# Optimization experiments

Hardware: AMD Instinct MI355X
Metric: run time of the kernel (lower is better)

## Reference

```python
import jax, jax.numpy as jnp
import numpy as np

B, S, D, H = 2, 2048, 1024, 16
HD = D // H
EPS = 1e-5


def setup_inputs() -> dict:
    key = jax.random.key(0)
    ks = jax.random.split(key, 11)
    sc = 0.02
    return {
        "x": jax.random.normal(ks[0], (B, S, D), jnp.float32),
        "wq": jax.random.normal(ks[1], (D, D), jnp.float32) * sc,
        "bq": jax.random.normal(ks[2], (D,), jnp.float32) * sc,
        "wk": jax.random.normal(ks[3], (D, D), jnp.float32) * sc,
        "bk": jax.random.normal(ks[4], (D,), jnp.float32) * sc,
        "wv": jax.random.normal(ks[5], (D, D), jnp.float32) * sc,
        "bv": jax.random.normal(ks[6], (D,), jnp.float32) * sc,
        "wo": jax.random.normal(ks[7], (D, D), jnp.float32) * sc,
        "bo": jax.random.normal(ks[8], (D,), jnp.float32) * sc,
        "gamma": 1.0 + jax.random.normal(ks[9], (D,), jnp.float32) * sc,
        "beta": jax.random.normal(ks[10], (D,), jnp.float32) * sc,
    }


def _layernorm(x, gamma, beta):
    mu = jnp.mean(x, axis=-1, keepdims=True)
    var = jnp.mean(jnp.square(x - mu), axis=-1, keepdims=True)
    return (x - mu) * jax.lax.rsqrt(var + EPS) * gamma + beta


def reference(x, wq, bq, wk, bk, wv, bv, wo, bo, gamma, beta):
    h = _layernorm(x, gamma, beta)
    # projections; torch Linear: y = x @ W.T + b
    q = (h @ wq.T + bq).reshape(B, S, H, HD).transpose(0, 2, 1, 3)  # [B,H,S,HD]
    k = (h @ wk.T + bk).reshape(B, S, H, HD).transpose(0, 2, 1, 3)
    v = (h @ wv.T + bv).reshape(B, S, H, HD).transpose(0, 2, 1, 3)
    # NOTE: original divides by sqrt(d_dim), not sqrt(head_dim)
    scores = jnp.einsum("bhqd,bhkd->bhqk", q, k) / np.sqrt(D).astype(np.float32)
    # faithful quirky causal masking: triu->transpose->softmax(dim=-2)->triu->transpose
    t = jnp.triu(scores).swapaxes(-2, -1)
    p = jax.nn.softmax(t, axis=-2)
    a = jnp.triu(p).swapaxes(-2, -1)  # [B,H,S,S]
    attn = jnp.einsum("bhqk,bhkd->bhqd", a, v)
    concat = attn.transpose(0, 2, 1, 3).reshape(B, S, D)
    return x + concat @ wo.T + bo
```

## Files before the change

kernel.cpp:

```cpp
#include <hip/hip_runtime.h>
#include <stdint.h>

typedef unsigned short u16;
typedef __bf16 bf8 __attribute__((ext_vector_type(8)));
typedef float f4 __attribute__((ext_vector_type(4)));

#define S_ 2048
#define D_ 1024
#define H_ 16
#define HD_ 64
#define M_ 4096

__device__ __forceinline__ u16 f2bf(float f) {
  union { float f; uint32_t u; } v; v.f = f;
  uint32_t u = v.u;
  u += 0x7FFF + ((u >> 16) & 1);
  return (u16)(u >> 16);
}

__device__ __forceinline__ float fexp2(float x) {
#if __has_builtin(__builtin_amdgcn_exp2f)
  return __builtin_amdgcn_exp2f(x);
#else
  float r; asm("v_exp_f32 %0, %1" : "=v"(r) : "v"(x)); return r;
#endif
}

__device__ __forceinline__ void load_lds16(const void* g, void* l) {
  __builtin_amdgcn_global_load_lds(
      (const __attribute__((address_space(1))) void*)g,
      (__attribute__((address_space(3))) void*)l, 16, 0, 0);
}

__device__ __forceinline__ void stage_ab(
    const u16* __restrict__ A, const u16* __restrict__ B,
    int m0, int n0, int kt, u16* buf, int tid) {
  #pragma unroll
  for (int l = 0; l < 4; ++l) {
    int p = l * 256 + tid;
    int q = p & 511;
    int row = q >> 2, c = q & 3;
    int clog = c ^ ((row >> 1) & 3);
    const u16* src = (p >> 9)
        ? (B + (size_t)(n0 + row) * 1024 + kt * 32 + clog * 8)
        : (A + (size_t)(m0 + row) * 1024 + kt * 32 + clog * 8);
    load_lds16(src, buf + p * 8);
  }
}

__global__ __launch_bounds__(256) void ln_kernel(
    const float* __restrict__ x, const float* __restrict__ gamma,
    const float* __restrict__ beta, u16* __restrict__ hbf) {
  int row = blockIdx.x;
  int tid = threadIdx.x;
  int w = tid >> 6, lane = tid & 63;
  const float* xr = x + (size_t)row * D_;
  float lv[4];
  float s = 0.f;
  #pragma unroll
  for (int i = 0; i < 4; ++i) { lv[i] = xr[tid + i * 256]; s += lv[i]; }
  __shared__ float red[8];
  #pragma unroll
  for (int off = 32; off >= 1; off >>= 1) s += __shfl_xor(s, off);
  if (lane == 0) red[w] = s;
  __syncthreads();
  float mean = (red[0] + red[1] + red[2] + red[3]) * (1.f / D_);
  float vs = 0.f;
  #pragma unroll
  for (int i = 0; i < 4; ++i) { float d = lv[i] - mean; vs += d * d; }
  #pragma unroll
  for (int off = 32; off >= 1; off >>= 1) vs += __shfl_xor(vs, off);
  if (lane == 0) red[4 + w] = vs;
  __syncthreads();
  float var = (red[4] + red[5] + red[6] + red[7]) * (1.f / D_);
  float rstd = rsqrtf(var + 1e-5f);
  #pragma unroll
  for (int i = 0; i < 4; ++i) {
    int col = tid + i * 256;
    float y = (lv[i] - mean) * rstd * gamma[col] + beta[col];
    hbf[(size_t)row * D_ + col] = f2bf(y);
  }
}

__global__ __launch_bounds__(256) void convw_kernel(
    const float* __restrict__ wq, const float* __restrict__ wk,
    const float* __restrict__ wv, const float* __restrict__ wo,
    u16* __restrict__ wqkv, u16* __restrict__ wobf, float* __restrict__ Z) {
  int i4 = blockIdx.x * 256 + threadIdx.x;
  int base = i4 * 4;
  int part = base >> 20;
  int off = base & 0xFFFFF;
  const float* src = part == 0 ? wq : part == 1 ? wk : part == 2 ? wv : wo;
  float4 v = *(const float4*)(src + off);
  ushort4 o;
  o.x = f2bf(v.x); o.y = f2bf(v.y); o.z = f2bf(v.z); o.w = f2bf(v.w);
  if (part < 3) *(ushort4*)(wqkv + base) = o;
  else *(ushort4*)(wobf + off) = o;
  if (i4 < 32 * S_) Z[i4] = (float)(i4 & (S_ - 1));
}

__global__ __launch_bounds__(256, 2) void gemm_qkv_kernel(
    const u16* __restrict__ A,
    const u16* __restrict__ W,
    const float* __restrict__ bq, const float* __restrict__ bk,
    const float* __restrict__ bv,
    u16* __restrict__ Qb, u16* __restrict__ Kb, float* __restrict__ Vf) {
  __shared__ u16 smem[4 * 8192];
  const int tid = threadIdx.x;
  const int w = tid >> 6, lane = tid & 63;
  const int wr = w >> 1, wc = w & 1;
  const int lr = lane & 15, hi = lane >> 4;
  const int kswz = (hi ^ ((lr >> 1) & 3)) * 8;

  int bid = blockIdx.x;
  int swz = (bid & 7) * 96 + (bid >> 3);
  const int m0 = (swz & 31) * 128;
  const int n0 = (swz >> 5) * 128;

  f4 acc[4][4];
  f4 zero = {0.f, 0.f, 0.f, 0.f};
  #pragma unroll
  for (int i = 0; i < 4; ++i)
    #pragma unroll
    for (int j = 0; j < 4; ++j) acc[i][j] = zero;

  stage_ab(A, W, m0, n0, 0, smem, tid);
  stage_ab(A, W, m0, n0, 1, smem + 8192, tid);
  stage_ab(A, W, m0, n0, 2, smem + 16384, tid);

  for (int t = 0; t < 32; ++t) {
    if (t < 30)      asm volatile("s_waitcnt vmcnt(8)\n\ts_barrier" ::: "memory");
    else if (t == 30) asm volatile("s_waitcnt vmcnt(4)\n\ts_barrier" ::: "memory");
    else             asm volatile("s_waitcnt vmcnt(0)\n\ts_barrier" ::: "memory");
    const u16* As = smem + (t & 3) * 8192;
    const u16* Bs = As + 4096;
    bf8 av[4], bvv[4];
    #pragma unroll
    for (int i = 0; i < 4; ++i)
      av[i] = *(const bf8*)&As[(wr * 64 + i * 16 + lr) * 32 + kswz];
    #pragma unroll
    for (int j = 0; j < 4; ++j)
      bvv[j] = *(const bf8*)&Bs[(wc * 64 + j * 16 + lr) * 32 + kswz];
    if (t < 29) stage_ab(A, W, m0, n0, t + 3, smem + ((t + 3) & 3) * 8192, tid);
    __builtin_amdgcn_s_setprio(1);
    #pragma unroll
    for (int i = 0; i < 4; ++i)
      #pragma unroll
      for (int j = 0; j < 4; ++j)
        acc[i][j] = __builtin_amdgcn_mfma_f32_16x16x32_bf16(
            av[i], bvv[j], acc[i][j], 0, 0, 0);
    __builtin_amdgcn_s_setprio(0);
  }

  const int part = n0 >> 10;
  const int colbase = n0 & 1023;
  const float SCQ = 0.04508422002778011f;
  if (part == 0) {
    #pragma unroll
    for (int i = 0; i < 4; ++i)
      #pragma unroll
      for (int j = 0; j < 4; ++j)
        #pragma unroll
        for (int r = 0; r < 4; ++r) {
          int m = m0 + wr * 64 + i * 16 + hi * 4 + r;
          int col = colbase + wc * 64 + j * 16 + lr;
          float val = (acc[i][j][r] + bq[col]) * SCQ;
          int b = m >> 11, s = m & 2047;
          int hh = col >> 6, d = col & 63;
          Qb[((size_t)(b * H_ + hh) * S_ + s) * HD_ + d] = f2bf(val);
        }
  } else if (part == 1) {
    #pragma unroll
    for (int i = 0; i < 4; ++i)
      #pragma unroll
      for (int j = 0; j < 4; ++j)
        #pragma unroll
        for (int r = 0; r < 4; ++r) {
          int m = m0 + wr * 64 + i * 16 + hi * 4 + r;
          int col = colbase + wc * 64 + j * 16 + lr;
          float val = acc[i][j][r] + bk[col];
          int b = m >> 11, s = m & 2047;
          int hh = col >> 6, d = col & 63;
          Kb[((size_t)(b * H_ + hh) * S_ + s) * HD_ + d] = f2bf(val);
        }
  } else {
    #pragma unroll
    for (int i = 0; i < 4; ++i)
      #pragma unroll
      for (int j = 0; j < 4; ++j)
        #pragma unroll
        for (int r = 0; r < 4; ++r) {
          int m = m0 + wr * 64 + i * 16 + hi * 4 + r;
          int col = colbase + wc * 64 + j * 16 + lr;
          float val = acc[i][j][r] + bv[col];
          int b = m >> 11, s = m & 2047;
          int hh = col >> 6, d = col & 63;
          Vf[((size_t)(b * H_ + hh) * S_ + s) * HD_ + d] = val;
        }
  }
}

__global__ __launch_bounds__(256, 4) void scores_z_kernel(
    const u16* __restrict__ Qb, const u16* __restrict__ Kb,
    float* __restrict__ Z, float* __restrict__ Ed) {
  int bid = blockIdx.x;
  int idx = bid >> 3;
  int bh = (bid & 7) * 4 + (idx / 144);
  int t = idx - (idx / 144) * 144;
  int g = 0;
  while (true) { int cnt = 4 * (8 - g); if (t < cnt) break; t -= cnt; ++g; }
  const int qb = g * 4 + (t & 3);
  const int c = g + (t >> 2);
  const bool diag = (c == g);

  const int tid = threadIdx.x;
  const int w = tid >> 6, lane = tid & 63;
  const int lr = lane & 15, hi = lane >> 4, lkb = hi * 8;
  const u16* Qh = Qb + (size_t)bh * S_ * HD_;
  const u16* Kh = Kb + (size_t)bh * S_ * HD_;
  const int q0 = qb * 64;

  bf8 a[4][2];
  #pragma unroll
  for (int g2 = 0; g2 < 4; ++g2) {
    a[g2][0] = *(const bf8*)&Qh[(q0 + g2 * 16 + lr) * 64 + lkb];
    a[g2][1] = *(const bf8*)&Qh[(q0 + g2 * 16 + lr) * 64 + 32 + lkb];
  }
  bf8 kb[4][2];
  #pragma unroll
  for (int i = 0; i < 4; ++i) {
    int kt = c * 16 + w + i * 4;
    kb[i][0] = *(const bf8*)&Kh[(kt * 16 + lr) * 64 + lkb];
    kb[i][1] = *(const bf8*)&Kh[(kt * 16 + lr) * 64 + 32 + lkb];
  }
  __builtin_amdgcn_sched_barrier(0);

  float zacc[4][4];
  #pragma unroll
  for (int g2 = 0; g2 < 4; ++g2)
    #pragma unroll
    for (int r = 0; r < 4; ++r) zacc[g2][r] = 0.f;

  #pragma unroll
  for (int i = 0; i < 4; ++i) {
    int kt = c * 16 + w + i * 4;
    int kcol = kt * 16 + lr;
    f4 cc[4];
    #pragma unroll
    for (int g2 = 0; g2 < 4; ++g2) {
      f4 z4 = {0.f, 0.f, 0.f, 0.f};
      z4 = __builtin_amdgcn_mfma_f32_16x16x32_bf16(a[g2][0], kb[i][0], z4, 0, 0, 0);
      cc[g2] = __builtin_amdgcn_mfma_f32_16x16x32_bf16(a[g2][1], kb[i][1], z4, 0, 0, 0);
    }
    if (diag) {
      #pragma unroll
      for (int g2 = 0; g2 < 4; ++g2) {
        #pragma unroll
        for (int r = 0; r < 4; ++r) {
          float e = fexp2(cc[g2][r]);
          int qrow = q0 + g2 * 16 + hi * 4 + r;
          zacc[g2][r] += (kcol >= qrow) ? e : 0.f;
          if (kcol == qrow) Ed[(size_t)bh * S_ + qrow] = e;
        }
      }
    } else {
      #pragma unroll
      for (int g2 = 0; g2 < 4; ++g2) {
        #pragma unroll
        for (int r = 0; r < 4; ++r)
          zacc[g2][r] += fexp2(cc[g2][r]);
      }
    }
  }

  __shared__ float Zp[4][64];
  #pragma unroll
  for (int g2 = 0; g2 < 4; ++g2) {
    #pragma unroll
    for (int r = 0; r < 4; ++r) {
      float v = zacc[g2][r];
      v += __shfl_xor(v, 1);
      v += __shfl_xor(v, 2);
      v += __shfl_xor(v, 4);
      v += __shfl_xor(v, 8);
      if (lr == 0) Zp[w][g2 * 16 + hi * 4 + r] = v;
    }
  }
  __syncthreads();
  if (tid < 64) {
    float z = Zp[0][tid] + Zp[1][tid] + Zp[2][tid] + Zp[3][tid];
    atomicAdd(&Z[(size_t)bh * S_ + q0 + tid], z);
  }
}

#define NC_ 128

__global__ __launch_bounds__(64) void vchunk_kernel(
    const float* __restrict__ Vf, float* __restrict__ csum) {
  int bh = blockIdx.y, c = blockIdx.x;
  int d = threadIdx.x;
  const float* vp = Vf + ((size_t)bh * S_ + c * 16) * HD_ + d;
  float s = 0.f;
  #pragma unroll
  for (int r = 0; r < 16; ++r) s += vp[r * HD_];
  csum[((size_t)bh * NC_ + c) * HD_ + d] = s;
}

__global__ __launch_bounds__(256) void vprefix_kernel(float* __restrict__ csum) {
  int bh = blockIdx.x;
  int d = threadIdx.x & 63;
  int qt = threadIdx.x >> 6;
  __shared__ float tot[4][64];
  float v[32];
  #pragma unroll
  for (int c = 0; c < 32; ++c)
    v[c] = csum[((size_t)bh * NC_ + qt * 32 + c) * HD_ + d];
  float run = 0.f;
  #pragma unroll
  for (int c = 0; c < 32; ++c) { float t = v[c]; v[c] = run; run += t; }
  tot[qt][d] = run;
  __syncthreads();
  float off = 0.f;
  #pragma unroll
  for (int p = 0; p < 4; ++p) if (p < qt) off += tot[p][d];
  #pragma unroll
  for (int c = 0; c < 32; ++c)
    csum[((size_t)bh * NC_ + qt * 32 + c) * HD_ + d] = v[c] + off;
}

__global__ __launch_bounds__(64) void attn_out_kernel(
    const float* __restrict__ Vf, const float* __restrict__ csum,
    const float* __restrict__ Z, const float* __restrict__ Ed,
    u16* __restrict__ concat) {
  int bh = blockIdx.y, c = blockIdx.x;
  int d = threadIdx.x;
  int b = bh >> 4, h = bh & 15;
  float run = csum[((size_t)bh * NC_ + c) * HD_ + d];
  #pragma unroll
  for (int r = 0; r < 16; ++r) {
    int s = c * 16 + r;
    size_t vi = ((size_t)bh * S_ + s) * HD_ + d;
    float v = Vf[vi];
    float z = Z[(size_t)bh * S_ + s];
    float e = Ed[(size_t)bh * S_ + s];
    float a = (run + e * v) / z;
    concat[(size_t)(b * S_ + s) * D_ + h * HD_ + d] = f2bf(a);
    run += v;
  }
}

__global__ __launch_bounds__(256, 2) void gemm_out_kernel(
    const u16* __restrict__ A,
    const u16* __restrict__ W,
    const float* __restrict__ x, const float* __restrict__ bo,
    float* __restrict__ out) {
  __shared__ u16 smem[4 * 8192];
  const int tid = threadIdx.x;
  const int w = tid >> 6, lane = tid & 63;
  const int wr = w >> 1, wc = w & 1;
  const int lr = lane & 15, hi = lane >> 4;
  const int kswz = (hi ^ ((lr >> 1) & 3)) * 8;

  int bid = blockIdx.x;
  int swz = (bid & 7) * 32 + (bid >> 3);
  const int m0 = (swz & 31) * 128;
  const int n0 = (swz >> 5) * 128;

  f4 acc[4][4];
  f4 zero = {0.f, 0.f, 0.f, 0.f};
  #pragma unroll
  for (int i = 0; i < 4; ++i)
    #pragma unroll
    for (int j = 0; j < 4; ++j) acc[i][j] = zero;

  stage_ab(A, W, m0, n0, 0, smem, tid);
  stage_ab(A, W, m0, n0, 1, smem + 8192, tid);
  stage_ab(A, W, m0, n0, 2, smem + 16384, tid);

  for (int t = 0; t < 32; ++t) {
    if (t < 30)      asm volatile("s_waitcnt vmcnt(8)\n\ts_barrier" ::: "memory");
    else if (t == 30) asm volatile("s_waitcnt vmcnt(4)\n\ts_barrier" ::: "memory");
    else             asm volatile("s_waitcnt vmcnt(0)\n\ts_barrier" ::: "memory");
    const u16* As = smem + (t & 3) * 8192;
    const u16* Bs = As + 4096;
    bf8 av[4], bvv[4];
    #pragma unroll
    for (int i = 0; i < 4; ++i)
      av[i] = *(const bf8*)&As[(wr * 64 + i * 16 + lr) * 32 + kswz];
    #pragma unroll
    for (int j = 0; j < 4; ++j)
      bvv[j] = *(const bf8*)&Bs[(wc * 64 + j * 16 + lr) * 32 + kswz];
    if (t < 29) stage_ab(A, W, m0, n0, t + 3, smem + ((t + 3) & 3) * 8192, tid);
    __builtin_amdgcn_s_setprio(1);
    #pragma unroll
    for (int i = 0; i < 4; ++i)
      #pragma unroll
      for (int j = 0; j < 4; ++j)
        acc[i][j] = __builtin_amdgcn_mfma_f32_16x16x32_bf16(
            av[i], bvv[j], acc[i][j], 0, 0, 0);
    __builtin_amdgcn_s_setprio(0);
  }

  #pragma unroll
  for (int i = 0; i < 4; ++i)
    #pragma unroll
    for (int j = 0; j < 4; ++j)
      #pragma unroll
      for (int r = 0; r < 4; ++r) {
        int m = m0 + wr * 64 + i * 16 + hi * 4 + r;
        int n = n0 + wc * 64 + j * 16 + lr;
        size_t oi = (size_t)m * D_ + n;
        out[oi] = x[oi] + acc[i][j][r] + bo[n];
      }
}

extern "C" void kernel_launch(void* const* d_in, const int* in_sizes, int n_in,
                              void* d_out, int out_size, void* d_ws, size_t ws_size,
                              hipStream_t stream) {
  (void)in_sizes; (void)n_in; (void)out_size; (void)ws_size;
  const float* x     = (const float*)d_in[0];
  const float* wq    = (const float*)d_in[1];
  const float* bq    = (const float*)d_in[2];
  const float* wk    = (const float*)d_in[3];
  const float* bk    = (const float*)d_in[4];
  const float* wv    = (const float*)d_in[5];
  const float* bv    = (const float*)d_in[6];
  const float* wo    = (const float*)d_in[7];
  const float* bo    = (const float*)d_in[8];
  const float* gamma = (const float*)d_in[9];
  const float* beta  = (const float*)d_in[10];
  float* out = (float*)d_out;

  char* ws = (char*)d_ws;
  u16* hbf    = (u16*)(ws);
  u16* wqkv   = (u16*)(ws + (8u << 20));
  u16* wobf   = (u16*)(ws + (14u << 20));
  u16* Qb     = (u16*)(ws + (16u << 20));
  u16* Kb     = (u16*)(ws + (24u << 20));
  float* Vf   = (float*)(ws + (32u << 20));
  float* Z    = (float*)(ws + (48u << 20));
  float* Ed   = (float*)(ws + (48u << 20) + (256u << 10));
  float* csum = (float*)(ws);
  u16* concat = (u16*)(ws + (16u << 20));

  ln_kernel<<<dim3(4096), dim3(256), 0, stream>>>(x, gamma, beta, hbf);
  convw_kernel<<<dim3(4096), dim3(256), 0, stream>>>(wq, wk, wv, wo, wqkv, wobf, Z);
  gemm_qkv_kernel<<<dim3(768), dim3(256), 0, stream>>>(hbf, wqkv, bq, bk, bv,
                                                       Qb, Kb, Vf);
  scores_z_kernel<<<dim3(4608), dim3(256), 0, stream>>>(Qb, Kb, Z, Ed);
  vchunk_kernel<<<dim3(NC_, 32), dim3(64), 0, stream>>>(Vf, csum);
  vprefix_kernel<<<dim3(32), dim3(256), 0, stream>>>(csum);
  attn_out_kernel<<<dim3(NC_, 32), dim3(64), 0, stream>>>(Vf, csum, Z, Ed, concat);
  gemm_out_kernel<<<dim3(256), dim3(256), 0, stream>>>(concat, wobf, x, bo, out);
}
```

Measured before the change: 210.0 us.

## Fuse prep kernels, store V as bf16, and retune GEMM pipelines and tile mapping

Merges the layernorm and weight-conversion kernels into one launch, which removes a kernel boundary. V is now stored as bf16 instead of fp32, halving its write and read traffic in the V-consuming kernels at some cost in precision. Both GEMMs move from a 4-stage to a 3-stage LDS ring with occupancy hint 3, and use a new XCD-aware block-to-tile mapping meant to improve L2 reuse. The shallower prefetch depth may expose more load latency.

```diff
diff --git a/kernel.cpp b/kernel.cpp
--- a/kernel.cpp
+++ b/kernel.cpp
@@ -16,6 +16,10 @@
   uint32_t u = v.u;
   u += 0x7FFF + ((u >> 16) & 1);
   return (u16)(u >> 16);
+}
+
+__device__ __forceinline__ float b2f(u16 u) {
+  union { uint32_t u; float f; } v; v.u = (uint32_t)u << 16; return v.f;
 }
 
 __device__ __forceinline__ float fexp2(float x) {
@@ -48,64 +52,64 @@
   }
 }
 
-__global__ __launch_bounds__(256) void ln_kernel(
+__global__ __launch_bounds__(256) void prep_kernel(
     const float* __restrict__ x, const float* __restrict__ gamma,
-    const float* __restrict__ beta, u16* __restrict__ hbf) {
-  int row = blockIdx.x;
-  int tid = threadIdx.x;
-  int w = tid >> 6, lane = tid & 63;
-  const float* xr = x + (size_t)row * D_;
-  float lv[4];
-  float s = 0.f;
-  #pragma unroll
-  for (int i = 0; i < 4; ++i) { lv[i] = xr[tid + i * 256]; s += lv[i]; }
-  __shared__ float red[8];
-  #pragma unroll
-  for (int off = 32; off >= 1; off >>= 1) s += __shfl_xor(s, off);
-  if (lane == 0) red[w] = s;
-  __syncthreads();
-  float mean = (red[0] + red[1] + red[2] + red[3]) * (1.f / D_);
-  float vs = 0.f;
-  #pragma unroll
-  for (int i = 0; i < 4; ++i) { float d = lv[i] - mean; vs += d * d; }
-  #pragma unroll
-  for (int off = 32; off >= 1; off >>= 1) vs += __shfl_xor(vs, off);
-  if (lane == 0) red[4 + w] = vs;
-  __syncthreads();
-  float var = (red[4] + red[5] + red[6] + red[7]) * (1.f / D_);
-  float rstd = rsqrtf(var + 1e-5f);
-  #pragma unroll
-  for (int i = 0; i < 4; ++i) {
-    int col = tid + i * 256;
-    float y = (lv[i] - mean) * rstd * gamma[col] + beta[col];
-    hbf[(size_t)row * D_ + col] = f2bf(y);
-  }
-}
-
-__global__ __launch_bounds__(256) void convw_kernel(
+    const float* __restrict__ beta, u16* __restrict__ hbf,
     const float* __restrict__ wq, const float* __restrict__ wk,
     const float* __restrict__ wv, const float* __restrict__ wo,
     u16* __restrict__ wqkv, u16* __restrict__ wobf, float* __restrict__ Z) {
-  int i4 = blockIdx.x * 256 + threadIdx.x;
-  int base = i4 * 4;
-  int part = base >> 20;
-  int off = base & 0xFFFFF;
-  const float* src = part == 0 ? wq : part == 1 ? wk : part == 2 ? wv : wo;
-  float4 v = *(const float4*)(src + off);
-  ushort4 o;
-  o.x = f2bf(v.x); o.y = f2bf(v.y); o.z = f2bf(v.z); o.w = f2bf(v.w);
-  if (part < 3) *(ushort4*)(wqkv + base) = o;
-  else *(ushort4*)(wobf + off) = o;
-  if (i4 < 32 * S_) Z[i4] = (float)(i4 & (S_ - 1));
-}
-
-__global__ __launch_bounds__(256, 2) void gemm_qkv_kernel(
+  int tid = threadIdx.x;
+  if (blockIdx.x < 4096) {
+    int row = blockIdx.x;
+    int w = tid >> 6, lane = tid & 63;
+    const float* xr = x + (size_t)row * D_;
+    float lv[4];
+    float s = 0.f;
+    #pragma unroll
+    for (int i = 0; i < 4; ++i) { lv[i] = xr[tid + i * 256]; s += lv[i]; }
+    __shared__ float red[8];
+    #pragma unroll
+    for (int off = 32; off >= 1; off >>= 1) s += __shfl_xor(s, off);
+    if (lane == 0) red[w] = s;
+    __syncthreads();
+    float mean = (red[0] + red[1] + red[2] + red[3]) * (1.f / D_);
+    float vs = 0.f;
+    #pragma unroll
+    for (int i = 0; i < 4; ++i) { float d = lv[i] - mean; vs += d * d; }
+    #pragma unroll
+    for (int off = 32; off >= 1; off >>= 1) vs += __shfl_xor(vs, off);
+    if (lane == 0) red[4 + w] = vs;
+    __syncthreads();
+    float var = (red[4] + red[5] + red[6] + red[7]) * (1.f / D_);
+    float rstd = rsqrtf(var + 1e-5f);
+    #pragma unroll
+    for (int i = 0; i < 4; ++i) {
+      int col = tid + i * 256;
+      float y = (lv[i] - mean) * rstd * gamma[col] + beta[col];
+      hbf[(size_t)row * D_ + col] = f2bf(y);
+    }
+  } else {
+    int i4 = (blockIdx.x - 4096) * 256 + tid;
+    int base = i4 * 4;
+    int part = base >> 20;
+    int off = base & 0xFFFFF;
+    const float* src = part == 0 ? wq : part == 1 ? wk : part == 2 ? wv : wo;
+    float4 v = *(const float4*)(src + off);
+    ushort4 o;
+    o.x = f2bf(v.x); o.y = f2bf(v.y); o.z = f2bf(v.z); o.w = f2bf(v.w);
+    if (part < 3) *(ushort4*)(wqkv + base) = o;
+    else *(ushort4*)(wobf + off) = o;
+    if (i4 < 32 * S_) Z[i4] = (float)(i4 & (S_ - 1));
+  }
+}
+
+__global__ __launch_bounds__(256, 3) void gemm_qkv_kernel(
     const u16* __restrict__ A,
     const u16* __restrict__ W,
     const float* __restrict__ bq, const float* __restrict__ bk,
     const float* __restrict__ bv,
-    u16* __restrict__ Qb, u16* __restrict__ Kb, float* __restrict__ Vf) {
-  __shared__ u16 smem[4 * 8192];
+    u16* __restrict__ Qb, u16* __restrict__ Kb, u16* __restrict__ Vb) {
+  __shared__ u16 smem[3 * 8192];
   const int tid = threadIdx.x;
   const int w = tid >> 6, lane = tid & 63;
   const int wr = w >> 1, wc = w & 1;
@@ -113,91 +117,63 @@
   const int kswz = (hi ^ ((lr >> 1) & 3)) * 8;
 
   int bid = blockIdx.x;
-  int swz = (bid & 7) * 96 + (bid >> 3);
-  const int m0 = (swz & 31) * 128;
-  const int n0 = (swz >> 5) * 128;
+  int xcd = bid & 7, i = bid >> 3;
+  int rc = xcd >> 2, cc = xcd & 3;
+  const int m0 = (rc * 16 + (i & 15)) * 128;
+  const int n0 = (cc * 6 + (i >> 4)) * 128;
 
   f4 acc[4][4];
   f4 zero = {0.f, 0.f, 0.f, 0.f};
   #pragma unroll
-  for (int i = 0; i < 4; ++i)
-    #pragma unroll
-    for (int j = 0; j < 4; ++j) acc[i][j] = zero;
+  for (int i2 = 0; i2 < 4; ++i2)
+    #pragma unroll
+    for (int j = 0; j < 4; ++j) acc[i2][j] = zero;
 
   stage_ab(A, W, m0, n0, 0, smem, tid);
   stage_ab(A, W, m0, n0, 1, smem + 8192, tid);
-  stage_ab(A, W, m0, n0, 2, smem + 16384, tid);
 
   for (int t = 0; t < 32; ++t) {
-    if (t < 30)      asm volatile("s_waitcnt vmcnt(8)\n\ts_barrier" ::: "memory");
-    else if (t == 30) asm volatile("s_waitcnt vmcnt(4)\n\ts_barrier" ::: "memory");
-    else             asm volatile("s_waitcnt vmcnt(0)\n\ts_barrier" ::: "memory");
-    const u16* As = smem + (t & 3) * 8192;
+    if (t < 31) asm volatile("s_waitcnt vmcnt(4)\n\ts_barrier" ::: "memory");
+    else        asm volatile("s_waitcnt vmcnt(0)\n\ts_barrier" ::: "memory");
+    const u16* As = smem + (t % 3) * 8192;
     const u16* Bs = As + 4096;
     bf8 av[4], bvv[4];
     #pragma unroll
-    for (int i = 0; i < 4; ++i)
-      av[i] = *(const bf8*)&As[(wr * 64 + i * 16 + lr) * 32 + kswz];
+    for (int i2 = 0; i2 < 4; ++i2)
+      av[i2] = *(const bf8*)&As[(wr * 64 + i2 * 16 + lr) * 32 + kswz];
     #pragma unroll
     for (int j = 0; j < 4; ++j)
       bvv[j] = *(const bf8*)&Bs[(wc * 64 + j * 16 + lr) * 32 + kswz];
-    if (t < 29) stage_ab(A, W, m0, n0, t + 3, smem + ((t + 3) & 3) * 8192, tid);
+    if (t < 30) stage_ab(A, W, m0, n0, t + 2, smem + ((t + 2) % 3) * 8192, tid);
     __builtin_amdgcn_s_setprio(1);
     #pragma unroll
-    for (int i = 0; i < 4; ++i)
+    for (int i2 = 0; i2 < 4; ++i2)
       #pragma unroll
       for (int j = 0; j < 4; ++j)
-        acc[i][j] = __builtin_amdgcn_mfma_f32_16x16x32_bf16(
-            av[i], bvv[j], acc[i][j], 0, 0, 0);
+        acc[i2][j] = __builtin_amdgcn_mfma_f32_16x16x32_bf16(
+            av[i2], bvv[j], acc[i2][j], 0, 0, 0);
     __builtin_amdgcn_s_setprio(0);
   }
 
   const int part = n0 >> 10;
   const int colbase = n0 & 1023;
   const float SCQ = 0.04508422002778011f;
-  if (part == 0) {
-    #pragma unroll
-    for (int i = 0; i < 4; ++i)
-      #pragma unroll
-      for (int j = 0; j < 4; ++j)
-        #pragma unroll
-        for (int r = 0; r < 4; ++r) {
-          int m = m0 + wr * 64 + i * 16 + hi * 4 + r;
-          int col = colbase + wc * 64 + j * 16 + lr;
-          float val = (acc[i][j][r] + bq[col]) * SCQ;
-          int b = m >> 11, s = m & 2047;
-          int hh = col >> 6, d = col & 63;
-          Qb[((size_t)(b * H_ + hh) * S_ + s) * HD_ + d] = f2bf(val);
-        }
-  } else if (part == 1) {
-    #pragma unroll
-    for (int i = 0; i < 4; ++i)
-      #pragma unroll
-      for (int j = 0; j < 4; ++j)
-        #pragma unroll
-        for (int r = 0; r < 4; ++r) {
-          int m = m0 + wr * 64 + i * 16 + hi * 4 + r;
-          int col = colbase + wc * 64 + j * 16 + lr;
-          float val = acc[i][j][r] + bk[col];
-          int b = m >> 11, s = m & 2047;
-          int hh = col >> 6, d = col & 63;
-          Kb[((size_t)(b * H_ + hh) * S_ + s) * HD_ + d] = f2bf(val);
-        }
-  } else {
-    #pragma unroll
-    for (int i = 0; i < 4; ++i)
-      #pragma unroll
-      for (int j = 0; j < 4; ++j)
-        #pragma unroll
-        for (int r = 0; r < 4; ++r) {
-          int m = m0 + wr * 64 + i * 16 + hi * 4 + r;
-          int col = colbase + wc * 64 + j * 16 + lr;
-          float val = acc[i][j][r] + bv[col];
-          int b = m >> 11, s = m & 2047;
-          int hh = col >> 6, d = col & 63;
-          Vf[((size_t)(b * H_ + hh) * S_ + s) * HD_ + d] = val;
-        }
-  }
+  const float* bias_p = part == 0 ? bq : (part == 1 ? bk : bv);
+  u16* dst = part == 0 ? Qb : (part == 1 ? Kb : Vb);
+  const float scale = part == 0 ? SCQ : 1.f;
+  #pragma unroll
+  for (int i2 = 0; i2 < 4; ++i2)
+    #pragma unroll
+    for (int j = 0; j < 4; ++j)
+      #pragma unroll
+      for (int r = 0; r < 4; ++r) {
+        int m = m0 + wr * 64 + i2 * 16 + hi * 4 + r;
+        int col = colbase + wc * 64 + j * 16 + lr;
+        float val = (acc[i2][j][r] + bias_p[col]) * scale;
+        int b = m >> 11, s = m & 2047;
+        int hh = col >> 6, d = col & 63;
+        dst[((size_t)(b * H_ + hh) * S_ + s) * HD_ + d] = f2bf(val);
+      }
 }
 
 __global__ __launch_bounds__(256, 4) void scores_z_kernel(
@@ -296,13 +272,13 @@
 #define NC_ 128
 
 __global__ __launch_bounds__(64) void vchunk_kernel(
-    const float* __restrict__ Vf, float* __restrict__ csum) {
+    const u16* __restrict__ Vb, float* __restrict__ csum) {
   int bh = blockIdx.y, c = blockIdx.x;
   int d = threadIdx.x;
-  const float* vp = Vf + ((size_t)bh * S_ + c * 16) * HD_ + d;
+  const u16* vp = Vb + ((size_t)bh * S_ + c * 16) * HD_ + d;
   float s = 0.f;
   #pragma unroll
-  for (int r = 0; r < 16; ++r) s += vp[r * HD_];
+  for (int r = 0; r < 16; ++r) s += b2f(vp[r * HD_]);
   csum[((size_t)bh * NC_ + c) * HD_ + d] = s;
 }
 
@@ -329,7 +305,7 @@
 }
 
 __global__ __launch_bounds__(64) void attn_out_kernel(
-    const float* __restrict__ Vf, const float* __restrict__ csum,
+    const u16* __restrict__ Vb, const float* __restrict__ csum,
     const float* __restrict__ Z, const float* __restrict__ Ed,
     u16* __restrict__ concat) {
   int bh = blockIdx.y, c = blockIdx.x;
@@ -339,8 +315,7 @@
   #pragma unroll
   for (int r = 0; r < 16; ++r) {
     int s = c * 16 + r;
-    size_t vi = ((size_t)bh * S_ + s) * HD_ + d;
-    float v = Vf[vi];
+    float v = b2f(Vb[((size_t)bh * S_ + s) * HD_ + d]);
     float z = Z[(size_t)bh * S_ + s];
     float e = Ed[(size_t)bh * S_ + s];
     float a = (run + e * v) / z;
@@ -349,12 +324,12 @@
   }
 }
 
-__global__ __launch_bounds__(256, 2) void gemm_out_kernel(
+__global__ __launch_bounds__(256, 3) void gemm_out_kernel(
     const u16* __restrict__ A,
     const u16* __restrict__ W,
     const float* __restrict__ x, const float* __restrict__ bo,
     float* __restrict__ out) {
-  __shared__ u16 smem[4 * 8192];
+  __shared__ u16 smem[3 * 8192];
   const int tid = threadIdx.x;
   const int w = tid >> 6, lane = tid & 63;
   const int wr = w >> 1, wc = w & 1;
@@ -362,55 +337,53 @@
   const int kswz = (hi ^ ((lr >> 1) & 3)) * 8;
 
   int bid = blockIdx.x;
-  int swz = (bid & 7) * 32 + (bid >> 3);
-  const int m0 = (swz & 31) * 128;
-  const int n0 = (swz >> 5) * 128;
+  int xcd = bid & 7, i = bid >> 3;
+  const int m0 = (xcd * 4 + (i & 3)) * 128;
+  const int n0 = (i >> 2) * 128;
 
   f4 acc[4][4];
   f4 zero = {0.f, 0.f, 0.f, 0.f};
   #pragma unroll
-  for (int i = 0; i < 4; ++i)
-    #pragma unroll
-    for (int j = 0; j < 4; ++j) acc[i][j] = zero;
+  for (int i2 = 0; i2 < 4; ++i2)
+    #pragma unroll
+    for (int j = 0; j < 4; ++j) acc[i2][j] = zero;
 
   stage_ab(A, W, m0, n0, 0, smem, tid);
   stage_ab(A, W, m0, n0, 1, smem + 8192, tid);
-  stage_ab(A, W, m0, n0, 2, smem + 16384, tid);
 
   for (int t = 0; t < 32; ++t) {
-    if (t < 30)      asm volatile("s_waitcnt vmcnt(8)\n\ts_barrier" ::: "memory");
-    else if (t == 30) asm volatile("s_waitcnt vmcnt(4)\n\ts_barrier" ::: "memory");
-    else             asm volatile("s_waitcnt vmcnt(0)\n\ts_barrier" ::: "memory");
-    const u16* As = smem + (t & 3) * 8192;
+    if (t < 31) asm volatile("s_waitcnt vmcnt(4)\n\ts_barrier" ::: "memory");
+    else        asm volatile("s_waitcnt vmcnt(0)\n\ts_barrier" ::: "memory");
+    const u16* As = smem + (t % 3) * 8192;
     const u16* Bs = As + 4096;
     bf8 av[4], bvv[4];
     #pragma unroll
-    for (int i = 0; i < 4; ++i)
-      av[i] = *(const bf8*)&As[(wr * 64 + i * 16 + lr) * 32 + kswz];
+    for (int i2 = 0; i2 < 4; ++i2)
+      av[i2] = *(const bf8*)&As[(wr * 64 + i2 * 16 + lr) * 32 + kswz];
     #pragma unroll
     for (int j = 0; j < 4; ++j)
       bvv[j] = *(const bf8*)&Bs[(wc * 64 + j * 16 + lr) * 32 + kswz];
-    if (t < 29) stage_ab(A, W, m0, n0, t + 3, smem + ((t + 3) & 3) * 8192, tid);
+    if (t < 30) stage_ab(A, W, m0, n0, t + 2, smem + ((t + 2) % 3) * 8192, tid);
     __builtin_amdgcn_s_setprio(1);
     #pragma unroll
-    for (int i = 0; i < 4; ++i)
+    for (int i2 = 0; i2 < 4; ++i2)
       #pragma unroll
       for (int j = 0; j < 4; ++j)
-        acc[i][j] = __builtin_amdgcn_mfma_f32_16x16x32_bf16(
-            av[i], bvv[j], acc[i][j], 0, 0, 0);
+        acc[i2][j] = __builtin_amdgcn_mfma_f32_16x16x32_bf16(
+            av[i2], bvv[j], acc[i2][j], 0, 0, 0);
     __builtin_amdgcn_s_setprio(0);
   }
 
   #pragma unroll
-  for (int i = 0; i < 4; ++i)
+  for (int i2 = 0; i2 < 4; ++i2)
     #pragma unroll
     for (int j = 0; j < 4; ++j)
       #pragma unroll
       for (int r = 0; r < 4; ++r) {
-        int m = m0 + wr * 64 + i * 16 + hi * 4 + r;
+        int m = m0 + wr * 64 + i2 * 16 + hi * 4 + r;
         int n = n0 + wc * 64 + j * 16 + lr;
         size_t oi = (size_t)m * D_ + n;
-        out[oi] = x[oi] + acc[i][j][r] + bo[n];
+        out[oi] = x[oi] + acc[i2][j][r] + bo[n];
       }
 }
 
@@ -437,19 +410,19 @@
   u16* wobf   = (u16*)(ws + (14u << 20));
   u16* Qb     = (u16*)(ws + (16u << 20));
   u16* Kb     = (u16*)(ws + (24u << 20));
-  float* Vf   = (float*)(ws + (32u << 20));
+  u16* Vb     = (u16*)(ws + (32u << 20));
   float* Z    = (float*)(ws + (48u << 20));
   float* Ed   = (float*)(ws + (48u << 20) + (256u << 10));
   float* csum = (float*)(ws);
   u16* concat = (u16*)(ws + (16u << 20));
 
-  ln_kernel<<<dim3(4096), dim3(256), 0, stream>>>(x, gamma, beta, hbf);
-  convw_kernel<<<dim3(4096), dim3(256), 0, stream>>>(wq, wk, wv, wo, wqkv, wobf, Z);
+  prep_kernel<<<dim3(8192), dim3(256), 0, stream>>>(
+      x, gamma, beta, hbf, wq, wk, wv, wo, wqkv, wobf, Z);
   gemm_qkv_kernel<<<dim3(768), dim3(256), 0, stream>>>(hbf, wqkv, bq, bk, bv,
-                                                       Qb, Kb, Vf);
+                                                       Qb, Kb, Vb);
   scores_z_kernel<<<dim3(4608), dim3(256), 0, stream>>>(Qb, Kb, Z, Ed);
-  vchunk_kernel<<<dim3(NC_, 32), dim3(64), 0, stream>>>(Vf, csum);
+  vchunk_kernel<<<dim3(NC_, 32), dim3(64), 0, stream>>>(Vb, csum);
   vprefix_kernel<<<dim3(32), dim3(256), 0, stream>>>(csum);
-  attn_out_kernel<<<dim3(NC_, 32), dim3(64), 0, stream>>>(Vf, csum, Z, Ed, concat);
+  attn_out_kernel<<<dim3(NC_, 32), dim3(64), 0, stream>>>(Vb, csum, Z, Ed, concat);
   gemm_out_kernel<<<dim3(256), dim3(256), 0, stream>>>(concat, wobf, x, bo, out);
 }
```

Result: faster. 199.8 us (-4.9%).
